# Optimization experiments

Measured on AMD Instinct MI355X. Metric: run time of the kernel, lower is better.

## Reference

```python
import jax, jax.numpy as jnp
import numpy as np

NA_CUTOFF = 30.0
OTHER_CUTOFF = 15.0
THRESHOLDS = jnp.array([0.5, 1.0, 2.0, 4.0], dtype=jnp.float32)


def _cdist(x):
    # x: [b, n, 3] -> [b, n, n] euclidean distances, safe-sqrt (0 grad at 0)
    diff = x[:, :, None, :] - x[:, None, :, :]
    sq = jnp.sum(diff * diff, axis=-1)
    safe = jnp.where(sq > 0, sq, 1.0)
    return jnp.where(sq > 0, jnp.sqrt(safe), 0.0)


def setup_inputs() -> dict:
    key = jax.random.key(0)
    k1, k2, k3, k4, k5 = jax.random.split(key, 5)
    b, n = 2, 4096
    # angstrom-scale coordinates so cutoffs (15/30 A) are meaningful
    true_coords = jax.random.normal(k1, (b, n, 3), dtype=jnp.float32) * 20.0
    pred_coords = true_coords + jax.random.normal(k2, (b, n, 3), dtype=jnp.float32) * 1.0
    is_dna = jax.random.randint(k3, (b, n), 0, 2) > 0
    is_rna = jax.random.randint(k4, (b, n), 0, 2) > 0
    coords_mask = jax.random.randint(k5, (b, n), 0, 2) > 0
    return {
        'pred_coords': pred_coords,
        'true_coords': true_coords,
        'is_dna': is_dna,
        'is_rna': is_rna,
        'coords_mask': coords_mask,
    }


def reference(pred_coords, true_coords, is_dna, is_rna, coords_mask):
    b, n, _ = pred_coords.shape
    pred_dists = _cdist(pred_coords)            # [b, n, n]
    true_dists = _cdist(true_coords)            # [b, n, n]
    dist_diff = jnp.abs(true_dists - pred_dists)
    # eps: sigmoid(threshold - |d_true - d_pred|), averaged over 4 thresholds
    eps = jax.nn.sigmoid(THRESHOLDS - dist_diff[..., None]).mean(axis=-1)  # [b, n, n]

    is_nt = is_dna | is_rna
    nt_pair = is_nt[:, :, None] & is_nt[:, None, :]
    inclusion = jnp.where(nt_pair, true_dists < NA_CUTOFF, true_dists < OTHER_CUTOFF)
    mask = inclusion & ~jnp.eye(n, dtype=bool)[None]
    mask = mask & (coords_mask[:, :, None] & coords_mask[:, None, :])

    maskf = mask.astype(eps.dtype)
    num = (eps * maskf).sum(axis=(-1, -2))
    den = jnp.maximum(maskf.sum(axis=(-1, -2)), 1.0)
    lddt = num / den
    return 1.0 - lddt.mean()
```

## Files before the change

### kernel.cpp

```cpp
#include <hip/hip_runtime.h>
#include <math.h>

#define NTHREADS 256
#define CAP 4096
#define NSBLK 544

#define LUTN 3072
#define OCT_LO (-16)
#define U_MIN 1.52587890625e-5f
#define U_MAX 255.999f
#define IDX_BYTE_BIAS 56832u

typedef float v2f __attribute__((ext_vector_type(2)));

__device__ __forceinline__ float fsqrt(float x) {
#if __has_builtin(__builtin_amdgcn_sqrtf)
    return __builtin_amdgcn_sqrtf(x);
#else
    return sqrtf(x);
#endif
}
__device__ __forceinline__ float fmed3(float x, float lo, float hi) {
#if __has_builtin(__builtin_amdgcn_fmed3f)
    return __builtin_amdgcn_fmed3f(x, lo, hi);
#else
    return fminf(fmaxf(x, lo), hi);
#endif
}

__device__ __forceinline__ float sig4(float d) {
    const float e = expf(d);
    return 1.0f / (1.0f + e * 0.60653065971263342360f)
         + 1.0f / (1.0f + e * 0.36787944117144232160f)
         + 1.0f / (1.0f + e * 0.13533528323661269189f)
         + 1.0f / (1.0f + e * 0.01831563888873418029f);
}

__global__ __launch_bounds__(256) void lut_build_kernel(float* __restrict__ gLUT) {
    const int e = blockIdx.x * 256 + threadIdx.x;
    if (e < LUTN) {
        const int oct = e >> 7;
        const int k   = e & 127;
        const float base2 = exp2f((float)(oct + OCT_LO));
        const float umid = base2 * (1.0f + ((float)k + 0.5f) * 0.0078125f);
        gLUT[e] = sig4(fsqrt(umid));
    }
}

__global__ __launch_bounds__(256) void compact_kernel(
    const float* __restrict__ pred, const float* __restrict__ tru,
    const int* __restrict__ dna, const int* __restrict__ rna,
    const int* __restrict__ cm,
    float* __restrict__ C, int* __restrict__ Mout, int n, int S )
{
    __shared__ int scan[256];
    const int b = blockIdx.x;
    const int tid = threadIdx.x;
    const size_t base = (size_t)b * n;
    const int npt = n / 256;

    int cnt = 0;
    unsigned int flags = 0;
    for (int k = 0; k < npt; ++k) {
        const int i = tid * npt + k;
        const int f = (cm[base + i] != 0) ? 1 : 0;
        flags |= (unsigned int)f << k;
        cnt += f;
    }
    scan[tid] = cnt;
    __syncthreads();
    for (int off = 1; off < 256; off <<= 1) {
        const int v = scan[tid];
        const int u = (tid >= off) ? scan[tid - off] : 0;
        __syncthreads();
        scan[tid] = v + u;
        __syncthreads();
    }
    const int M = scan[255];
    int pos = scan[tid] - cnt;
    if (tid == 0) Mout[b] = M;

    float* cpx = C + 0 * S + b * CAP;  float* cpy = C + 1 * S + b * CAP;
    float* cpz = C + 2 * S + b * CAP;  float* ctx = C + 3 * S + b * CAP;
    float* cty = C + 4 * S + b * CAP;  float* ctz = C + 5 * S + b * CAP;
    float* ccn = C + 6 * S + b * CAP;  float* cco = C + 7 * S + b * CAP;
    float* cnt_f = C + 8 * S + b * CAP;

    for (int k = 0; k < npt; ++k) {
        if ((flags >> k) & 1u) {
            const int i = tid * npt + k;
            const float* p = pred + (base + i) * 3;
            const float* q = tru  + (base + i) * 3;
            const int nt = (dna[base + i] != 0) || (rna[base + i] != 0);
            cpx[pos] = p[0]; cpy[pos] = p[1]; cpz[pos] = p[2];
            ctx[pos] = q[0]; cty[pos] = q[1]; ctz[pos] = q[2];
            ccn[pos] = nt ? 900.0f : 225.0f;
            cco[pos] = 225.0f;
            cnt_f[pos] = nt ? 1.0f : 0.0f;
            ++pos;
        }
    }
    for (int k = M + tid; k < CAP; k += 256) {
        cpx[k] = 1.0e9f; cpy[k] = 1.0e9f; cpz[k] = 1.0e9f;
        ctx[k] = 1.0e9f; cty[k] = 1.0e9f; ctz[k] = 1.0e9f;
        ccn[k] = 0.0f; cco[k] = 0.0f; cnt_f[k] = 0.0f;
    }
}

__device__ __forceinline__ void pair_tail(float sqp, float sqt, float cut2,
                                          const char* __restrict__ lutB,
                                          float& num, float& den) {
    const float r  = fsqrt(sqt * sqp);
    const float u0 = fmaf(-2.0f, r, sqt + sqp);
    const float u  = fmed3(u0, U_MIN, U_MAX);
    const unsigned int bits = __float_as_uint(u);
    const float s  = *(const float*)(lutB + ((bits >> 14) & ~3u));
    const float m  = (sqt < cut2) ? 1.0f : 0.0f;
    num = fmaf(m, s, num);
    den += m;
}

__global__ __launch_bounds__(NTHREADS) void lddt_tile_kernel(
    const float* __restrict__ C, const int* __restrict__ Mptr,
    const float* __restrict__ gLUT,
    float* __restrict__ pnum, float* __restrict__ pden, int S)
{
    __shared__ __align__(16) float sPX[256], sPY[256], sPZ[256];
    __shared__ __align__(16) float sTX[256], sTY[256], sTZ[256];
    __shared__ __align__(16) float sCut[2 * 256];
    __shared__ __align__(16) float sLUT[LUTN];
    __shared__ float wnum[4], wden[4];

    const int tid = threadIdx.x;

    int s = blockIdx.x;
    const int bi = s / NSBLK;
    s -= bi * NSBLK;
    const int q = s >> 2;
    const int r = s & 3;
    const int W = 33;
    int g = (int)(((float)W - fsqrt((float)(W * W - 8 * q))) * 0.5f);
    while ((g + 1) * 16 - ((g + 1) * g) / 2 <= q) ++g;
    while (g * 16 - (g * (g - 1)) / 2 > q) --g;
    const int sc = g + (q - (g * 16 - (g * (g - 1)) / 2));
    const int ti = 4 * g + r;
    const int i0 = 64 * ti;
    const int J0 = 256 * sc;
    const bool has_diag = (sc == g);
    const int M = Mptr[bi];

    if (i0 >= M || J0 >= M) {
        if (tid == 0) { pnum[blockIdx.x] = 0.0f; pden[blockIdx.x] = 0.0f; }
        return;
    }

    const int bo = bi * CAP;
    const float* cpx = C + 0 * S + bo;  const float* cpy = C + 1 * S + bo;
    const float* cpz = C + 2 * S + bo;  const float* ctx = C + 3 * S + bo;
    const float* cty = C + 4 * S + bo;  const float* ctz = C + 5 * S + bo;
    const float* ccn = C + 6 * S + bo;  const float* cco = C + 7 * S + bo;
    const float* cntf = C + 8 * S + bo;

    {
        const float4* gl4 = (const float4*)gLUT;
        float4* sl4 = (float4*)sLUT;
        #pragma unroll
        for (int e = tid; e < LUTN / 4; e += NTHREADS) sl4[e] = gl4[e];
    }

    {
        const int j = J0 + tid;
        sPX[tid] = cpx[j]; sPY[tid] = cpy[j]; sPZ[tid] = cpz[j];
        sTX[tid] = ctx[j]; sTY[tid] = cty[j]; sTZ[tid] = ctz[j];
        sCut[tid] = ccn[j]; sCut[256 + tid] = cco[j];
    }

    const int w = tid >> 6;
    const int l = tid & 63;
    const int i = i0 + l;
    const float pix = cpx[i], piy = cpy[i], piz = cpz[i];
    const float tix = ctx[i], tiy = cty[i], tiz = ctz[i];
    const bool nti = (cntf[i] != 0.0f);
    __syncthreads();

    const float* cutsel = nti ? &sCut[0] : &sCut[256];
    const char* lutB = (const char*)sLUT - IDX_BYTE_BIAS;
    const int kbase = 16 * w;

    const v2f px2 = {pix, pix}, py2 = {piy, piy}, pz2 = {piz, piz};
    const v2f tx2 = {tix, tix}, ty2 = {tiy, tiy}, tz2 = {tiz, tiz};

    float accn = 0.0f, accd = 0.0f;

    #pragma unroll
    for (int c = 0; c < 4; ++c) {
        const int tj = 4 * sc + c;
        if (tj < ti || 64 * tj >= M) continue;
        const bool diag = has_diag && (c == r);
        const int o = 64 * c;

        float num = 0.0f, den = 0.0f;
        #pragma unroll
        for (int qd = 0; qd < 4; ++qd) {
            const int jq = o + kbase + 4 * qd;
            const float4 PX = *(const float4*)&sPX[jq];
            const float4 PY = *(const float4*)&sPY[jq];
            const float4 PZ = *(const float4*)&sPZ[jq];
            const float4 TX = *(const float4*)&sTX[jq];
            const float4 TY = *(const float4*)&sTY[jq];
            const float4 TZ = *(const float4*)&sTZ[jq];
            const float4 CTC = *(const float4*)&cutsel[jq];

            v2f dx, dy, dz, sqpA, sqpB, sqtA, sqtB;

            dx = px2 - (v2f){PX.x, PX.y}; dy = py2 - (v2f){PY.x, PY.y}; dz = pz2 - (v2f){PZ.x, PZ.y};
            sqpA = dx * dx + dy * dy + dz * dz;
            dx = tx2 - (v2f){TX.x, TX.y}; dy = ty2 - (v2f){TY.x, TY.y}; dz = tz2 - (v2f){TZ.x, TZ.y};
            sqtA = dx * dx + dy * dy + dz * dz;

            dx = px2 - (v2f){PX.z, PX.w}; dy = py2 - (v2f){PY.z, PY.w}; dz = pz2 - (v2f){PZ.z, PZ.w};
            sqpB = dx * dx + dy * dy + dz * dz;
            dx = tx2 - (v2f){TX.z, TX.w}; dy = ty2 - (v2f){TY.z, TY.w}; dz = tz2 - (v2f){TZ.z, TZ.w};
            sqtB = dx * dx + dy * dy + dz * dz;

            pair_tail(sqpA.x, sqtA.x, CTC.x, lutB, num, den);
            pair_tail(sqpA.y, sqtA.y, CTC.y, lutB, num, den);
            pair_tail(sqpB.x, sqtB.x, CTC.z, lutB, num, den);
            pair_tail(sqpB.y, sqtB.y, CTC.w, lutB, num, den);
        }
        const float sc2 = diag ? 1.0f : 2.0f;
        accn = fmaf(sc2, num, accn);
        accd = fmaf(sc2, den, accd);
    }

    if (has_diag && ((l >> 4) == w) && i < M) {
        accn -= sLUT[0];
        accd -= 1.0f;
    }

    #pragma unroll
    for (int off = 32; off > 0; off >>= 1) {
        accn += __shfl_down(accn, off, 64);
        accd += __shfl_down(accd, off, 64);
    }
    if ((tid & 63) == 0) { wnum[w] = accn; wden[w] = accd; }
    __syncthreads();

    if (tid == 0) {
        pnum[blockIdx.x] = wnum[0] + wnum[1] + wnum[2] + wnum[3];
        pden[blockIdx.x] = wden[0] + wden[1] + wden[2] + wden[3];
    }
}

__global__ __launch_bounds__(256) void lddt_final_kernel(
    const float* __restrict__ pnum, const float* __restrict__ pden,
    float* __restrict__ out, int nsblk)
{
    __shared__ double sn0[4], sn1[4], sd0[4], sd1[4];
    double n0 = 0, n1 = 0, d0 = 0, d1 = 0;
    for (int s = threadIdx.x; s < 2 * nsblk; s += 256) {
        if (s < nsblk) { n0 += (double)pnum[s]; d0 += (double)pden[s]; }
        else           { n1 += (double)pnum[s]; d1 += (double)pden[s]; }
    }
    #pragma unroll
    for (int off = 32; off > 0; off >>= 1) {
        n0 += __shfl_down(n0, off, 64); d0 += __shfl_down(d0, off, 64);
        n1 += __shfl_down(n1, off, 64); d1 += __shfl_down(d1, off, 64);
    }
    const int w = threadIdx.x >> 6;
    if ((threadIdx.x & 63) == 0) { sn0[w] = n0; sn1[w] = n1; sd0[w] = d0; sd1[w] = d1; }
    __syncthreads();
    if (threadIdx.x == 0) {
        double N0 = sn0[0] + sn0[1] + sn0[2] + sn0[3];
        double N1 = sn1[0] + sn1[1] + sn1[2] + sn1[3];
        double D0 = sd0[0] + sd0[1] + sd0[2] + sd0[3];
        double D1 = sd1[0] + sd1[1] + sd1[2] + sd1[3];
        D0 = D0 > 1.0 ? D0 : 1.0;
        D1 = D1 > 1.0 ? D1 : 1.0;
        const double l0 = 0.25 * N0 / D0;
        const double l1 = 0.25 * N1 / D1;
        out[0] = (float)(1.0 - 0.5 * (l0 + l1));
    }
}

extern "C" void kernel_launch(void* const* d_in, const int* in_sizes, int n_in,
                              void* d_out, int out_size, void* d_ws, size_t ws_size,
                              hipStream_t stream) {
    const float* pred = (const float*)d_in[0];
    const float* tru  = (const float*)d_in[1];
    const int*   dna  = (const int*)d_in[2];
    const int*   rna  = (const int*)d_in[3];
    const int*   cm   = (const int*)d_in[4];
    float* out = (float*)d_out;

    const int B = 2;
    const int n = in_sizes[2] / B;
    const int S = B * CAP;

    char* p = (char*)d_ws;
    float* gLUT = (float*)p;                 p += (size_t)LUTN * sizeof(float);
    float* C    = (float*)p;                 p += (size_t)9 * S * sizeof(float);
    float* pnum = (float*)p;                 p += (size_t)B * NSBLK * sizeof(float);
    float* pden = (float*)p;                 p += (size_t)B * NSBLK * sizeof(float);
    int*   Mout = (int*)p;

    hipLaunchKernelGGL(lut_build_kernel, dim3((LUTN + 255) / 256), dim3(256), 0, stream,
                       gLUT);
    hipLaunchKernelGGL(compact_kernel, dim3(B), dim3(256), 0, stream,
                       pred, tru, dna, rna, cm, C, Mout, n, S);
    hipLaunchKernelGGL(lddt_tile_kernel, dim3(B * NSBLK), dim3(NTHREADS), 0, stream,
                       C, Mout, gLUT, pnum, pden, S);
    hipLaunchKernelGGL(lddt_final_kernel, dim3(1), dim3(256), 0, stream,
                       pnum, pden, out, NSBLK);
}
```

Measured before the change: 93.39 us.

## Parallelize compaction across chunks with atomic offsets and prefill padding

The compaction kernel previously ran on one block per batch and walked 16 elements per thread serially. It now launches one block per 256-element chunk, scans within the block, and reserves output slots with an atomicAdd on a per-batch counter. Padding is no longer written after compaction: the LUT build kernel, renamed prep, now also fills the whole buffer with padding values and zeroes the counters. Because chunks append in arbitrary order, the compacted order changes between runs, which can make the floating-point reduction non-deterministic.

```diff
diff --git a/kernel.cpp b/kernel.cpp
--- a/kernel.cpp
+++ b/kernel.cpp
@@ -36,39 +36,42 @@
          + 1.0f / (1.0f + e * 0.01831563888873418029f);
 }
 
-__global__ __launch_bounds__(256) void lut_build_kernel(float* __restrict__ gLUT) {
-    const int e = blockIdx.x * 256 + threadIdx.x;
-    if (e < LUTN) {
-        const int oct = e >> 7;
-        const int k   = e & 127;
+__global__ __launch_bounds__(256) void prep_kernel(
+    float* __restrict__ gLUT, float* __restrict__ C, int* __restrict__ Mcnt, int S)
+{
+    const int gid = blockIdx.x * 256 + threadIdx.x;
+    if (gid < LUTN) {
+        const int oct = gid >> 7;
+        const int k   = gid & 127;
         const float base2 = exp2f((float)(oct + OCT_LO));
         const float umid = base2 * (1.0f + ((float)k + 0.5f) * 0.0078125f);
-        gLUT[e] = sig4(fsqrt(umid));
-    }
+        gLUT[gid] = sig4(fsqrt(umid));
+    }
+    if (gid < 2) Mcnt[gid] = 0;
+    const int total = 9 * S;
+    const int stride = gridDim.x * 256;
+    for (int idx = gid; idx < total; idx += stride)
+        C[idx] = (idx < 6 * S) ? 1.0e9f : 0.0f;
 }
 
 __global__ __launch_bounds__(256) void compact_kernel(
     const float* __restrict__ pred, const float* __restrict__ tru,
     const int* __restrict__ dna, const int* __restrict__ rna,
     const int* __restrict__ cm,
-    float* __restrict__ C, int* __restrict__ Mout, int n, int S )
+    float* __restrict__ C, int* __restrict__ Mcnt, int n, int S)
 {
     __shared__ int scan[256];
-    const int b = blockIdx.x;
+    __shared__ int sbase;
+    const int chunks = n / 256;
+    const int b = blockIdx.x / chunks;
+    const int chunk = blockIdx.x % chunks;
     const int tid = threadIdx.x;
-    const size_t base = (size_t)b * n;
-    const int npt = n / 256;
-
-    int cnt = 0;
-    unsigned int flags = 0;
-    for (int k = 0; k < npt; ++k) {
-        const int i = tid * npt + k;
-        const int f = (cm[base + i] != 0) ? 1 : 0;
-        flags |= (unsigned int)f << k;
-        cnt += f;
-    }
-    scan[tid] = cnt;
-    __syncthreads();
+    const size_t gi = (size_t)b * n + chunk * 256 + tid;
+
+    const int f = (cm[gi] != 0) ? 1 : 0;
+    scan[tid] = f;
+    __syncthreads();
+    #pragma unroll
     for (int off = 1; off < 256; off <<= 1) {
         const int v = scan[tid];
         const int u = (tid >= off) ? scan[tid - off] : 0;
@@ -76,34 +79,21 @@
         scan[tid] = v + u;
         __syncthreads();
     }
-    const int M = scan[255];
-    int pos = scan[tid] - cnt;
-    if (tid == 0) Mout[b] = M;
-
-    float* cpx = C + 0 * S + b * CAP;  float* cpy = C + 1 * S + b * CAP;
-    float* cpz = C + 2 * S + b * CAP;  float* ctx = C + 3 * S + b * CAP;
-    float* cty = C + 4 * S + b * CAP;  float* ctz = C + 5 * S + b * CAP;
-    float* ccn = C + 6 * S + b * CAP;  float* cco = C + 7 * S + b * CAP;
-    float* cnt_f = C + 8 * S + b * CAP;
-
-    for (int k = 0; k < npt; ++k) {
-        if ((flags >> k) & 1u) {
-            const int i = tid * npt + k;
-            const float* p = pred + (base + i) * 3;
-            const float* q = tru  + (base + i) * 3;
-            const int nt = (dna[base + i] != 0) || (rna[base + i] != 0);
-            cpx[pos] = p[0]; cpy[pos] = p[1]; cpz[pos] = p[2];
-            ctx[pos] = q[0]; cty[pos] = q[1]; ctz[pos] = q[2];
-            ccn[pos] = nt ? 900.0f : 225.0f;
-            cco[pos] = 225.0f;
-            cnt_f[pos] = nt ? 1.0f : 0.0f;
-            ++pos;
-        }
-    }
-    for (int k = M + tid; k < CAP; k += 256) {
-        cpx[k] = 1.0e9f; cpy[k] = 1.0e9f; cpz[k] = 1.0e9f;
-        ctx[k] = 1.0e9f; cty[k] = 1.0e9f; ctz[k] = 1.0e9f;
-        ccn[k] = 0.0f; cco[k] = 0.0f; cnt_f[k] = 0.0f;
+    if (tid == 255) sbase = atomicAdd(&Mcnt[b], scan[255]);
+    __syncthreads();
+
+    if (f) {
+        const int pos = sbase + scan[tid] - 1;
+        const float* p = pred + gi * 3;
+        const float* q = tru  + gi * 3;
+        const int nt = (dna[gi] != 0) || (rna[gi] != 0);
+        const int bo = b * CAP;
+        C[0 * S + bo + pos] = p[0];  C[1 * S + bo + pos] = p[1];
+        C[2 * S + bo + pos] = p[2];  C[3 * S + bo + pos] = q[0];
+        C[4 * S + bo + pos] = q[1];  C[5 * S + bo + pos] = q[2];
+        C[6 * S + bo + pos] = nt ? 900.0f : 225.0f;
+        C[7 * S + bo + pos] = 225.0f;
+        C[8 * S + bo + pos] = nt ? 1.0f : 0.0f;
     }
 }
 
@@ -167,7 +157,6 @@
         #pragma unroll
         for (int e = tid; e < LUTN / 4; e += NTHREADS) sl4[e] = gl4[e];
     }
-
     {
         const int j = J0 + tid;
         sPX[tid] = cpx[j]; sPY[tid] = cpy[j]; sPZ[tid] = cpz[j];
@@ -302,14 +291,14 @@
     float* C    = (float*)p;                 p += (size_t)9 * S * sizeof(float);
     float* pnum = (float*)p;                 p += (size_t)B * NSBLK * sizeof(float);
     float* pden = (float*)p;                 p += (size_t)B * NSBLK * sizeof(float);
-    int*   Mout = (int*)p;
-
-    hipLaunchKernelGGL(lut_build_kernel, dim3((LUTN + 255) / 256), dim3(256), 0, stream,
-                       gLUT);
-    hipLaunchKernelGGL(compact_kernel, dim3(B), dim3(256), 0, stream,
-                       pred, tru, dna, rna, cm, C, Mout, n, S);
+    int*   Mcnt = (int*)p;
+
+    hipLaunchKernelGGL(prep_kernel, dim3(288), dim3(256), 0, stream,
+                       gLUT, C, Mcnt, S);
+    hipLaunchKernelGGL(compact_kernel, dim3(B * (n / 256)), dim3(256), 0, stream,
+                       pred, tru, dna, rna, cm, C, Mcnt, n, S);
     hipLaunchKernelGGL(lddt_tile_kernel, dim3(B * NSBLK), dim3(NTHREADS), 0, stream,
-                       C, Mout, gLUT, pnum, pden, S);
+                       C, Mcnt, gLUT, pnum, pden, S);
     hipLaunchKernelGGL(lddt_final_kernel, dim3(1), dim3(256), 0, stream,
                        pnum, pden, out, NSBLK);
 }
```

After: 76.76 us (median of 2 runs). -17.8%, faster.
